# Optimization experiments

Measured on AMD Instinct MI355X. Metric: run time of the kernel, lower is better.

The kernel has to match this reference:

```python
import jax, jax.numpy as jnp
import numpy as np

N_NODES = 16500   # 100 battles x 165 hexes
N_EDGES = 100000  # per link type
K = 3             # number of link types (HeteroConv branches)
C_IN, C_HID, C_OUT = 170, 256, 256
GEN_EPS = 1e-7    # GENConv eps
BN_EPS = 1e-5     # BatchNorm1d eps


def setup_inputs() -> dict:
    key = jax.random.key(0)
    ki = iter(jax.random.split(key, 32))
    inp = {}
    inp["x"] = jax.random.normal(next(ki), (N_NODES, C_IN), jnp.float32)
    inp["edge_index"] = jax.random.randint(next(ki), (K, 2, N_EDGES), 0, N_NODES, dtype=jnp.int32)
    inp["edge_attr"] = jax.random.normal(next(ki), (K, N_EDGES, 1), jnp.float32)

    def uni(k, fan_in, shape):
        b = float(1.0 / np.sqrt(fan_in))
        return jax.random.uniform(k, shape, jnp.float32, -b, b)

    dims = [(C_IN, C_HID), (C_HID, C_HID), (C_HID, C_OUT)]
    for l, (ci, co) in enumerate(dims):
        inp[f"We{l}"] = uni(next(ki), 1, (K, 1, ci))          # edge encoder Linear(1, ci)
        inp[f"be{l}"] = jnp.zeros((K, ci), jnp.float32)
        inp[f"Wa{l}"] = uni(next(ki), ci, (K, ci, 2 * ci))     # MLP layer 1 (expansion=2)
        inp[f"ba{l}"] = jnp.zeros((K, 2 * ci), jnp.float32)
        inp[f"g{l}"] = jnp.ones((K, 2 * ci), jnp.float32)      # BatchNorm gamma
        inp[f"bt{l}"] = jnp.zeros((K, 2 * ci), jnp.float32)    # BatchNorm beta
        inp[f"Wb{l}"] = uni(next(ki), 2 * ci, (K, 2 * ci, co)) # MLP layer 2
        inp[f"bb{l}"] = jnp.zeros((K, co), jnp.float32)
    return inp


def _genconv(x, src, dst, ea, We, be, Wa, ba, g, bt, Wb, bb):
    """PyG GENConv (aggr='softmax', t=1, eps=1e-7, norm='batch') with self loops."""
    n = x.shape[0]
    loops = jnp.arange(n, dtype=src.dtype)
    src = jnp.concatenate([src, loops])
    dst = jnp.concatenate([dst, loops])
    ea = jnp.concatenate([ea, jnp.ones((n, ea.shape[1]), ea.dtype)], axis=0)
    e = ea @ We + be                           # [E+N, ci] edge encoder
    msg = jax.nn.relu(x[src] + e) + GEN_EPS    # [E+N, ci] message
    # per-destination, per-channel segment softmax aggregation
    mx = jax.ops.segment_max(msg, dst, num_segments=n)
    w = jnp.exp(msg - mx[dst])
    den = jax.ops.segment_sum(w, dst, num_segments=n)
    aggr = jax.ops.segment_sum(msg * w, dst, num_segments=n) / den
    out = aggr + x                             # residual with root node
    # MLP: Linear -> BatchNorm(train stats) -> ReLU -> Linear
    h = out @ Wa + ba
    mu = h.mean(axis=0)
    var = ((h - mu) ** 2).mean(axis=0)
    h = (h - mu) * jax.lax.rsqrt(var + BN_EPS) * g + bt
    h = jax.nn.relu(h)
    return h @ Wb + bb


_conv_k = jax.vmap(_genconv, in_axes=(None, 0, 0, 0, 0, 0, 0, 0, 0, 0, 0, 0))


def _forward(x, edge_index, edge_attr, layers):
    h = x
    for i, p in enumerate(layers):
        # HeteroConv: run GENConv per link type, sum-aggregate over types
        h = _conv_k(h, edge_index[:, 0], edge_index[:, 1], edge_attr, *p).sum(axis=0)
        if i < len(layers) - 1:
            h = jax.nn.leaky_relu(h, 0.01)
    return h


def reference(x, edge_index, edge_attr,
              We0, be0, Wa0, ba0, g0, bt0, Wb0, bb0,
              We1, be1, Wa1, ba1, g1, bt1, Wb1, bb1,
              We2, be2, Wa2, ba2, g2, bt2, Wb2, bb2):
    layers = [(We0, be0, Wa0, ba0, g0, bt0, Wb0, bb0),
              (We1, be1, Wa1, ba1, g1, bt1, Wb1, bb1),
              (We2, be2, Wa2, ba2, g2, bt2, Wb2, bb2)]
    return _forward(x, edge_index, edge_attr, layers)
```

## Files before the change

kernel.cpp:

```cpp
#include <hip/hip_runtime.h>
#include <math.h>

#define NN 16500
#define NP 16512
#define NE 100000
#define KT 3

typedef __attribute__((ext_vector_type(8))) short bf8_t;
typedef __attribute__((ext_vector_type(4))) float f4_t;

__device__ __forceinline__ unsigned short f2bf(float f) {
    unsigned int u = __float_as_uint(f);
    u += 0x7fffu + ((u >> 16) & 1u);
    return (unsigned short)(u >> 16);
}
__device__ __forceinline__ float bf2f(unsigned short h) {
    return __uint_as_float(((unsigned int)h) << 16);
}
__device__ __forceinline__ void gload16(unsigned short* lds, const unsigned short* g) {
    __builtin_amdgcn_global_load_lds(
        (const __attribute__((address_space(1))) void*)g,
        (__attribute__((address_space(3))) void*)lds, 16, 0, 0);
}


__global__ void deg_kernel(const int* __restrict__ ei, int* __restrict__ deg) {
    int t = blockIdx.x * blockDim.x + threadIdx.x;
    if (t >= KT * NE) return;
    int k = t / NE, e = t - k * NE;
    int d = ei[k * 2 * NE + NE + e];
    atomicAdd(&deg[k * NN + d], 1);
}

__global__ void scan_kernel(const int* __restrict__ deg, int* __restrict__ offs,
                            int* __restrict__ cursor) {
    int k = blockIdx.x;
    const int* dg = deg + k * NN;
    int* of = offs + k * (NN + 1);
    int* cu = cursor + k * NN;
    __shared__ int part[256];
    int tid = threadIdx.x;
    const int chunk = (NN + 255) / 256;
    int s0 = tid * chunk, s1 = min(NN, s0 + chunk);
    if (s0 > s1) s0 = s1;
    int sum = 0;
    for (int i = s0; i < s1; ++i) sum += dg[i];
    part[tid] = sum;
    __syncthreads();
    for (int off = 1; off < 256; off <<= 1) {
        int v = part[tid];
        int vp = (tid >= off) ? part[tid - off] : 0;
        __syncthreads();
        part[tid] = v + vp;
        __syncthreads();
    }
    int run = (tid == 0) ? 0 : part[tid - 1];
    for (int i = s0; i < s1; ++i) {
        of[i] = run; cu[i] = run;
        run += dg[i];
    }
    if (tid == 255) of[NN] = run;
}

__global__ void scatter_kernel(const int* __restrict__ ei, const float* __restrict__ ea,
                               int* __restrict__ cursor, int2* __restrict__ se) {
    int t = blockIdx.x * blockDim.x + threadIdx.x;
    if (t >= KT * NE) return;
    int k = t / NE, e = t - k * NE;
    int s = ei[k * 2 * NE + e];
    int d = ei[k * 2 * NE + NE + e];
    float a = ea[(size_t)k * NE + e];
    int pos = atomicAdd(&cursor[k * NN + d], 1);
    int2 p; p.x = s; p.y = __float_as_int(a);
    se[(size_t)k * NE + pos] = p;
}


template<int CI, bool BF16X>
__device__ __forceinline__ void loadrow4(float out[4], const void* xv, int s, int c0) {
    if (BF16X) {
        const unsigned short* xb = (const unsigned short*)xv;
        uint2 u = *(const uint2*)(xb + (size_t)s * CI + c0);
        out[0] = bf2f((unsigned short)(u.x & 0xffffu));
        out[1] = bf2f((unsigned short)(u.x >> 16));
        out[2] = bf2f((unsigned short)(u.y & 0xffffu));
        out[3] = bf2f((unsigned short)(u.y >> 16));
    } else {
        const float* p = (const float*)xv + (size_t)s * CI + c0;
        if (c0 + 4 <= CI) {
            float2 ab = *(const float2*)p;
            float2 cd = *(const float2*)(p + 2);
            out[0] = ab.x; out[1] = ab.y; out[2] = cd.x; out[3] = cd.y;
        } else {
            #pragma unroll
            for (int e = 0; e < 4; ++e) out[e] = (c0 + e < CI) ? p[e] : 0.f;
        }
    }
}

template<int CI, bool BF16X>
__global__ __launch_bounds__(256) void aggr_kernel(
    const void* __restrict__ xv, const int2* __restrict__ se_all,
    const int* __restrict__ offs_all,
    const float* __restrict__ We_all, const float* __restrict__ be_all,
    unsigned short* __restrict__ out_hi)
{
    constexpr int KP = (CI + 31) / 32 * 32;
    int k = blockIdx.y;
    int wv = threadIdx.x >> 6, lane = threadIdx.x & 63;
    int c0 = lane * 4;
    unsigned short* o = out_hi + (size_t)k * NP * KP;
    const int2*  se   = se_all + (size_t)k * NE;
    const int*   offs = offs_all + k * (NN + 1);
    const float* We   = We_all + (size_t)k * CI;
    const float* be   = be_all + (size_t)k * CI;

    constexpr bool ACT_ALL = (64 * 4 == KP) && (CI == KP);
    bool act = ACT_ALL || (c0 < CI);
    float w[4], b[4];
    #pragma unroll
    for (int e = 0; e < 4; ++e) {
        bool a = (c0 + e) < CI;
        w[e] = a ? We[c0 + e] : 0.f;
        b[e] = a ? be[c0 + e] : 0.f;
    }

    for (int it = 0; it < 4; ++it) {
        int d = blockIdx.x * 16 + it * 4 + wv;
        if (d >= NN) {
            if (c0 < KP) { uint2 z = {0u, 0u}; *(uint2*)(o + (size_t)d * KP + c0) = z; }
            continue;
        }
        float xd[4] = {0.f, 0.f, 0.f, 0.f};
        if (act) loadrow4<CI, BF16X>(xd, xv, d, c0);
        #pragma unroll
        for (int e = 0; e < 4; ++e) if ((c0 + e) >= CI) xd[e] = 0.f;

        float den[4], num[4];
        #pragma unroll
        for (int e = 0; e < 4; ++e) {
            float mg = fmaxf(xd[e] + w[e] + b[e], 0.f);
            float ex = __expf(mg);
            den[e] = ex;
            num[e] = mg * ex;
        }

        auto step = [&](const float xc[4], float a) {
            #pragma unroll
            for (int e = 0; e < 4; ++e) {
                float t = xc[e] + fmaf(a, w[e], b[e]);
                float mg = fmaxf(t, 0.f);
                float ex = __expf(mg);
                den[e] += ex;
                num[e] = fmaf(mg, ex, num[e]);
            }
        };

        int start = offs[d], end = offs[d + 1];
        for (int base = start; base < end; base += 64) {
            int cnt = min(64, end - base);
            int sv = 0; float av = 0.f;
            if (lane < cnt) {
                int2 p = se[base + lane];
                sv = p.x; av = __int_as_float(p.y);
            }
            float x0[4] = {0.f,0.f,0.f,0.f}, x1[4] = {0.f,0.f,0.f,0.f};
            float x2[4] = {0.f,0.f,0.f,0.f}, x3[4] = {0.f,0.f,0.f,0.f};
            {
                int sA = __shfl(sv, 0), sB = __shfl(sv, 1);
                int sC = __shfl(sv, 2), sD = __shfl(sv, 3);
                if (act)            loadrow4<CI, BF16X>(x0, xv, sA, c0);
                if (act && cnt > 1) loadrow4<CI, BF16X>(x1, xv, sB, c0);
                if (act && cnt > 2) loadrow4<CI, BF16X>(x2, xv, sC, c0);
                if (act && cnt > 3) loadrow4<CI, BF16X>(x3, xv, sD, c0);
            }
            int j = 0;
            for (; j + 3 < cnt; j += 4) {
                float a0 = __shfl(av, j),     a1 = __shfl(av, j + 1);
                float a2 = __shfl(av, j + 2), a3 = __shfl(av, j + 3);
                int s4 = __shfl(sv, (j + 4) & 63), s5 = __shfl(sv, (j + 5) & 63);
                int s6 = __shfl(sv, (j + 6) & 63), s7 = __shfl(sv, (j + 7) & 63);
                step(x0, a0);
                if (act && (j + 4) < cnt) loadrow4<CI, BF16X>(x0, xv, s4, c0);
                step(x1, a1);
                if (act && (j + 5) < cnt) loadrow4<CI, BF16X>(x1, xv, s5, c0);
                step(x2, a2);
                if (act && (j + 6) < cnt) loadrow4<CI, BF16X>(x2, xv, s6, c0);
                step(x3, a3);
                if (act && (j + 7) < cnt) loadrow4<CI, BF16X>(x3, xv, s7, c0);
            }
            if (j < cnt)     step(x0, __shfl(av, j));
            if (j + 1 < cnt) step(x1, __shfl(av, j + 1));
            if (j + 2 < cnt) step(x2, __shfl(av, j + 2));
        }
        if (c0 < KP) {
            unsigned short r[4];
            #pragma unroll
            for (int e = 0; e < 4; ++e) {
                float v = ((c0 + e) < CI) ? (num[e] / den[e] + xd[e]) : 0.f;
                r[e] = f2bf(v);
            }
            uint2 pk = {(unsigned)r[0] | ((unsigned)r[1] << 16),
                        (unsigned)r[2] | ((unsigned)r[3] << 16)};
            *(uint2*)(o + (size_t)d * KP + c0) = pk;
        }
    }
}


struct SplitJob { const float* W; unsigned short* out; int kdim, ndim, np_, kp; };
struct SplitJobs { SplitJob j[6]; };

__global__ void split_all_kernel(SplitJobs jobs) {
    SplitJob jb = jobs.j[blockIdx.z];
    int idx = blockIdx.x * 256 + threadIdx.x;
    int total = KT * jb.np_ * jb.kp;
    if (idx >= total) return;
    int k = idx / (jb.np_ * jb.kp);
    int rem = idx - k * jb.np_ * jb.kp;
    int n = rem / jb.kp;
    int kk = rem - n * jb.kp;
    float v = (n < jb.ndim && kk < jb.kdim) ? jb.W[((size_t)k * jb.kdim + kk) * jb.ndim + n] : 0.f;
    jb.out[idx] = f2bf(v);
}


__global__ __launch_bounds__(256, 3) void gemm1_mfma(
    const unsigned short* __restrict__ A_hi,
    const unsigned short* __restrict__ B_hi,
    const float* __restrict__ bias_all, unsigned short* __restrict__ C_all,
    float* __restrict__ psum,
    int KP, int ldc, int Mv, int Nv)
{
    __shared__ unsigned short Ah[2][128 * 32];
    __shared__ unsigned short Bh[2][128 * 32];

    int z = blockIdx.z;
    int gxT = gridDim.x, gyT = gridDim.y;
    int NHP = gxT * 128;
    const unsigned short* Ahg = A_hi + (size_t)z * NP * KP;
    const unsigned short* Bhg = B_hi + (size_t)z * NHP * KP;
    const float* bias = bias_all + (size_t)z * Nv;
    unsigned short* C = C_all + (size_t)z * NP * ldc;

    int tid = threadIdx.x;
    int w = tid >> 6, l = tid & 63;
    int bm = blockIdx.y * 128, bn = blockIdx.x * 128;
    int lane15 = l & 15, quad = l >> 4;
    int wm = (w >> 1) * 64, wn = (w & 1) * 64;
    int srow = l & 15;
    int scol = (l >> 4) * 8;

    f4_t acc[4][4];
    #pragma unroll
    for (int i = 0; i < 4; ++i)
        #pragma unroll
        for (int j = 0; j < 4; ++j) { f4_t zz = {0.f,0.f,0.f,0.f}; acc[i][j] = zz; }

    size_t aoff0 = (size_t)(bm + 32 * w +  0 + srow) * KP + scol;
    size_t aoff1 = (size_t)(bm + 32 * w + 16 + srow) * KP + scol;
    size_t boff0 = (size_t)(bn + 32 * w +  0 + srow) * KP + scol;
    size_t boff1 = (size_t)(bn + 32 * w + 16 + srow) * KP + scol;
    int rb0 = 32 * w, rb1 = 32 * w + 16;
    int ta = (w >> 1) * 4, tb = (w & 1) * 4;

    gload16(&Ah[0][rb0 * 32], Ahg + aoff0);
    gload16(&Ah[0][rb1 * 32], Ahg + aoff1);
    gload16(&Bh[0][rb0 * 32], Bhg + boff0);
    gload16(&Bh[0][rb1 * 32], Bhg + boff1);
    __syncthreads();

    int cur = 0;
    for (int k0 = 32; k0 < KP; k0 += 32) {
        int nxt = cur ^ 1;
        gload16(&Ah[nxt][rb0 * 32], Ahg + aoff0 + k0);
        gload16(&Ah[nxt][rb1 * 32], Ahg + aoff1 + k0);
        gload16(&Bh[nxt][rb0 * 32], Bhg + boff0 + k0);
        gload16(&Bh[nxt][rb1 * 32], Bhg + boff1 + k0);

        bf8_t fa[4], fb[4];
        #pragma unroll
        for (int i = 0; i < 4; ++i) {
            fa[i] = *(const bf8_t*)&Ah[cur][(ta + i) * 512 + l * 8];
            fb[i] = *(const bf8_t*)&Bh[cur][(tb + i) * 512 + l * 8];
        }
        #pragma unroll
        for (int i = 0; i < 4; ++i)
            #pragma unroll
            for (int j = 0; j < 4; ++j)
                acc[i][j] = __builtin_amdgcn_mfma_f32_16x16x32_bf16(fa[i], fb[j], acc[i][j], 0, 0, 0);
        __syncthreads();
        cur = nxt;
    }
    {
        bf8_t fa[4], fb[4];
        #pragma unroll
        for (int i = 0; i < 4; ++i) {
            fa[i] = *(const bf8_t*)&Ah[cur][(ta + i) * 512 + l * 8];
            fb[i] = *(const bf8_t*)&Bh[cur][(tb + i) * 512 + l * 8];
        }
        #pragma unroll
        for (int i = 0; i < 4; ++i)
            #pragma unroll
            for (int j = 0; j < 4; ++j)
                acc[i][j] = __builtin_amdgcn_mfma_f32_16x16x32_bf16(fa[i], fb[j], acc[i][j], 0, 0, 0);
    }

    #pragma unroll
    for (int j = 0; j < 4; ++j) {
        int c = bn + wn + j * 16 + lane15;
        float bc = (c < Nv) ? bias[c] : 0.f;
        float s1 = 0.f, s2 = 0.f;
        #pragma unroll
        for (int i = 0; i < 4; ++i) {
            #pragma unroll
            for (int r5 = 0; r5 < 4; ++r5) {
                int r = bm + wm + i * 16 + quad * 4 + r5;
                float v = acc[i][j][r5] + bc;
                unsigned short q = f2bf(v);
                if (r < Mv && c < Nv) C[(size_t)r * ldc + c] = q;
                bool ok = (r < NN) && (c < Nv);
                float vq = ok ? bf2f(q) : 0.f;
                s1 += vq;
                s2 = fmaf(vq, vq, s2);
            }
        }
        s1 += __shfl_xor(s1, 16); s2 += __shfl_xor(s2, 16);
        s1 += __shfl_xor(s1, 32); s2 += __shfl_xor(s2, 32);
        if (quad == 0) {
            int wrow = w >> 1;
            int col = wn + j * 16 + lane15;
            size_t o = ((((size_t)z * gyT + blockIdx.y) * gxT + blockIdx.x) * 2 + wrow) * 256 + col * 2;
            float2 st = {s1, s2};
            *(float2*)&psum[o] = st;
        }
    }
}


__global__ __launch_bounds__(256) void finalize_kernel(
    const float* __restrict__ psum,
    const float* __restrict__ g_all, const float* __restrict__ bt_all,
    float* __restrict__ scale_all, float* __restrict__ shift_all,
    int hid, int gxT)
{
    int z = blockIdx.x;
    int t64 = threadIdx.x & 63;
    int slice = threadIdx.x >> 6;
    int c = blockIdx.y * 64 + t64;
    __shared__ double rs1[4][64];
    __shared__ double rs2[4][64];
    double s1 = 0.0, s2 = 0.0;
    if (c < gxT * 128) {
        int gx = c >> 7, col = c & 127;
        for (int gy = slice; gy < NP / 128; gy += 4) {
            size_t base = (((size_t)z * (NP / 128) + gy) * gxT + gx) * 2 * 256 + col * 2;
            float2 a  = *(const float2*)&psum[base];
            float2 b2 = *(const float2*)&psum[base + 256];
            s1 += (double)a.x + b2.x;
            s2 += (double)a.y + b2.y;
        }
    }
    rs1[slice][t64] = s1;
    rs2[slice][t64] = s2;
    __syncthreads();
    if (slice == 0 && c < hid) {
        double S1 = rs1[0][t64] + rs1[1][t64] + rs1[2][t64] + rs1[3][t64];
        double S2 = rs2[0][t64] + rs2[1][t64] + rs2[2][t64] + rs2[3][t64];
        double mu = S1 / NN;
        double var = S2 / NN - mu * mu;
        if (var < 0.0) var = 0.0;
        float rs = (float)(1.0 / sqrt(var + 1e-5));
        float sc = rs * g_all[(size_t)z * hid + c];
        scale_all[(size_t)z * 512 + c] = sc;
        shift_all[(size_t)z * 512 + c] = bt_all[(size_t)z * hid + c] - (float)mu * sc;
    }
}


__device__ __forceinline__ bf8_t bnpack(uint4 hv, float4 s0, float4 s1,
                                        float4 t0, float4 t1, int ch0, int hid) {
    unsigned int uu[4] = {hv.x, hv.y, hv.z, hv.w};
    float ss[8] = {s0.x, s0.y, s0.z, s0.w, s1.x, s1.y, s1.z, s1.w};
    float tt[8] = {t0.x, t0.y, t0.z, t0.w, t1.x, t1.y, t1.z, t1.w};
    bf8_t r;
    #pragma unroll
    for (int e = 0; e < 8; ++e) {
        unsigned short hb = (e & 1) ? (unsigned short)(uu[e >> 1] >> 16)
                                    : (unsigned short)(uu[e >> 1] & 0xffffu);
        float x = bf2f(hb);
        float val = (ch0 + e < hid) ? fmaxf(fmaf(x, ss[e], tt[e]), 0.f) : 0.f;
        r[e] = (short)f2bf(val);
    }
    return r;
}

__global__ __launch_bounds__(256, 2) void gemm2_mfma(
    const unsigned short* __restrict__ h_all, const float* __restrict__ scale_all,
    const float* __restrict__ shift_all,
    const unsigned short* __restrict__ B_hi,
    const float* __restrict__ bb,
    float* __restrict__ outf, unsigned short* __restrict__ outb,
    int KP, int hid, int leaky, int as_bf16)
{
    __shared__ unsigned short Ah[2][64 * 32];
    __shared__ unsigned short Bh[2][128 * 32];

    int tid = threadIdx.x;
    int w = tid >> 6, l = tid & 63;
    int bm = blockIdx.y * 64, bn = blockIdx.x * 128;
    int lane15 = l & 15, quad = l >> 4;
    int wm = (w >> 1) * 32, wn = (w & 1) * 64;
    int srow = l & 15, scol = (l >> 4) * 8;

    const int KPZ = KP / 32;
    const int NIT = 3 * KPZ;

    f4_t acc[2][4];
    #pragma unroll
    for (int i = 0; i < 2; ++i)
        #pragma unroll
        for (int j = 0; j < 4; ++j) { f4_t zz = {0.f,0.f,0.f,0.f}; acc[i][j] = zz; }

    int rb0 = 32 * w, rb1 = 32 * w + 16;
    int ta = (w >> 1) * 2, tb = (w & 1) * 4;
    int grow = ((tid >> 6) << 4) + (tid & 15);
    int ccol = ((tid >> 4) & 3) * 8;

    size_t arow = (size_t)(bm + grow) * KP + ccol;
    size_t brow0 = (size_t)(bn + 32 * w + srow) * KP + scol;
    size_t brow1 = (size_t)(bn + 32 * w + 16 + srow) * KP + scol;

    {
        uint4 hv = *(const uint4*)(h_all + arow);
        gload16(&Bh[0][rb0 * 32], B_hi + brow0);
        gload16(&Bh[0][rb1 * 32], B_hi + brow1);
        const float* scl = scale_all + ccol;
        const float* shf = shift_all + ccol;
        float4 s0 = *(const float4*)scl, s1 = *(const float4*)(scl + 4);
        float4 t0 = *(const float4*)shf, t1 = *(const float4*)(shf + 4);
        *(bf8_t*)&Ah[0][tid * 8] = bnpack(hv, s0, s1, t0, t1, ccol, hid);
    }
    __syncthreads();

    int cur = 0;
    for (int it = 0; it < NIT; ++it) {
        int nit = it + 1;
        bool have = nit < NIT;
        int nxt = cur ^ 1;
        uint4 hv;
        float4 s0, s1, t0, t1;
        int nch = 0;
        if (have) {
            int nzz = nit / KPZ, nkk = (nit - nzz * KPZ) * 32;
            nch = nkk + ccol;
            hv = *(const uint4*)(h_all + (size_t)nzz * NP * KP + arow + nkk);
            const float* scl = scale_all + (size_t)nzz * 512 + nch;
            const float* shf = shift_all + (size_t)nzz * 512 + nch;
            s0 = *(const float4*)scl; s1 = *(const float4*)(scl + 4);
            t0 = *(const float4*)shf; t1 = *(const float4*)(shf + 4);
            const unsigned short* bz = B_hi + (size_t)nzz * 256 * KP + nkk;
            gload16(&Bh[nxt][rb0 * 32], bz + brow0);
            gload16(&Bh[nxt][rb1 * 32], bz + brow1);
        }
        bf8_t fa[2], fb[4];
        #pragma unroll
        for (int i = 0; i < 2; ++i)
            fa[i] = *(const bf8_t*)&Ah[cur][(ta + i) * 512 + l * 8];
        #pragma unroll
        for (int j = 0; j < 4; ++j)
            fb[j] = *(const bf8_t*)&Bh[cur][(tb + j) * 512 + l * 8];
        #pragma unroll
        for (int i = 0; i < 2; ++i)
            #pragma unroll
            for (int j = 0; j < 4; ++j)
                acc[i][j] = __builtin_amdgcn_mfma_f32_16x16x32_bf16(fa[i], fb[j], acc[i][j], 0, 0, 0);
        if (have)
            *(bf8_t*)&Ah[nxt][tid * 8] = bnpack(hv, s0, s1, t0, t1, nch, hid);
        __syncthreads();
        cur = nxt;
    }

    #pragma unroll
    for (int j = 0; j < 4; ++j) {
        int c = bn + wn + j * 16 + lane15;
        float bsum = bb[c] + bb[256 + c] + bb[512 + c];
        #pragma unroll
        for (int i = 0; i < 2; ++i) {
            #pragma unroll
            for (int r5 = 0; r5 < 4; ++r5) {
                int r = bm + wm + i * 16 + quad * 4 + r5;
                if (r < NN) {
                    float v = acc[i][j][r5] + bsum;
                    if (leaky) v = (v > 0.f) ? v : 0.01f * v;
                    if (as_bf16) outb[(size_t)r * 256 + c] = f2bf(v);
                    else         outf[(size_t)r * 256 + c] = v;
                }
            }
        }
    }
}


extern "C" void kernel_launch(void* const* d_in, const int* in_sizes, int n_in,
                              void* d_out, int out_size, void* d_ws, size_t ws_size,
                              hipStream_t stream)
{
    const float* x  = (const float*)d_in[0];
    const int*   ei = (const int*)d_in[1];
    const float* ea = (const float*)d_in[2];

    char* w = (char*)d_ws;
    auto alloc = [&](size_t bytes) {
        char* p = w;
        w += (bytes + 255) & ~(size_t)255;
        return p;
    };
    int* deg    = (int*)alloc((size_t)KT * NN * 4);
    int* offs   = (int*)alloc((size_t)KT * (NN + 1) * 4);
    int* cursor = (int*)alloc((size_t)KT * NN * 4);
    int2* se    = (int2*)alloc((size_t)KT * NE * 8);
    unsigned short* a1_hi = (unsigned short*)alloc((size_t)KT * NP * 256 * 2);
    unsigned short* h3 = (unsigned short*)alloc((size_t)KT * NP * 512 * 2);
    unsigned short* bta_l[3];
    unsigned short* btb_l[3];
    for (int l = 0; l < 3; ++l) {
        bta_l[l] = (unsigned short*)alloc((size_t)KT * 512 * 256 * 2);
        btb_l[l] = (unsigned short*)alloc((size_t)KT * 256 * 512 * 2);
    }
    float* psum = (float*)alloc((size_t)KT * (NP / 128) * 4 * 2 * 256 * 4);
    float* scale3 = (float*)alloc((size_t)KT * 512 * 4);
    float* shift3 = (float*)alloc((size_t)KT * 512 * 4);
    unsigned short* bufA = (unsigned short*)alloc((size_t)NN * 256 * 2);
    unsigned short* bufB = (unsigned short*)alloc((size_t)NN * 256 * 2);

    hipMemsetAsync(deg, 0, (size_t)KT * NN * 4, stream);
    int net = KT * NE;
    deg_kernel<<<(net + 255) / 256, 256, 0, stream>>>(ei, deg);
    scan_kernel<<<KT, 256, 0, stream>>>(deg, offs, cursor);
    scatter_kernel<<<(net + 255) / 256, 256, 0, stream>>>(ei, ea, cursor, se);

    SplitJobs jobs;
    int maxtot = 0;
    for (int l = 0; l < 3; ++l) {
        int ci  = (l == 0) ? 170 : 256;
        int KP1 = (ci + 31) / 32 * 32;
        int hid = 2 * ci;
        int NHP = (hid + 127) / 128 * 128;
        int KP2 = (hid + 31) / 32 * 32;
        jobs.j[2 * l]     = { (const float*)d_in[3 + 8 * l + 2], bta_l[l], ci,  hid, NHP, KP1 };
        jobs.j[2 * l + 1] = { (const float*)d_in[3 + 8 * l + 6], btb_l[l], hid, 256, 256, KP2 };
        maxtot = max(maxtot, KT * NHP * KP1);
        maxtot = max(maxtot, KT * 256 * KP2);
    }
    dim3 gsp((maxtot + 255) / 256, 1, 6);
    split_all_kernel<<<gsp, 256, 0, stream>>>(jobs);

    const void* hin = x;
    for (int l = 0; l < 3; ++l) {
        int ci  = (l == 0) ? 170 : 256;
        int KP1 = (ci + 31) / 32 * 32;
        int hid = 2 * ci;
        int NHP = (hid + 127) / 128 * 128;
        int KP2 = (hid + 31) / 32 * 32;
        const float* We = (const float*)d_in[3 + 8 * l + 0];
        const float* be = (const float*)d_in[3 + 8 * l + 1];
        const float* ba = (const float*)d_in[3 + 8 * l + 3];
        const float* g  = (const float*)d_in[3 + 8 * l + 4];
        const float* bt = (const float*)d_in[3 + 8 * l + 5];
        const float* bb = (const float*)d_in[3 + 8 * l + 7];

        dim3 ga(NP / 16, KT);
        if (l == 0)
            aggr_kernel<170, false><<<ga, 256, 0, stream>>>(hin, se, offs, We, be, a1_hi);
        else
            aggr_kernel<256, true><<<ga, 256, 0, stream>>>(hin, se, offs, We, be, a1_hi);

        dim3 g1(NHP / 128, NP / 128, KT);
        gemm1_mfma<<<g1, 256, 0, stream>>>(a1_hi, bta_l[l], ba, h3, psum, KP1, KP2, NN, hid);

        dim3 gf(KT, 8);
        finalize_kernel<<<gf, 256, 0, stream>>>(psum, g, bt, scale3, shift3, hid, NHP / 128);

        unsigned short* outb = (l == 0) ? bufA : bufB;
        dim3 g2(2, NP / 64);
        gemm2_mfma<<<g2, 256, 0, stream>>>(h3, scale3, shift3, btb_l[l], bb,
                                           (float*)d_out, outb, KP2, hid,
                                           (l < 2) ? 1 : 0, (l < 2) ? 1 : 0);

        hin = (l < 2) ? (const void*)outb : nullptr;
    }
}
```

Baseline: 671.2 us.

## Replace LDS-staged GEMM tiles with direct register loads of MFMA fragments

```diff
diff --git a/kernel.cpp b/kernel.cpp
--- a/kernel.cpp
+++ b/kernel.cpp
@@ -16,11 +16,6 @@
 }
 __device__ __forceinline__ float bf2f(unsigned short h) {
     return __uint_as_float(((unsigned int)h) << 16);
-}
-__device__ __forceinline__ void gload16(unsigned short* lds, const unsigned short* g) {
-    __builtin_amdgcn_global_load_lds(
-        (const __attribute__((address_space(1))) void*)g,
-        (__attribute__((address_space(3))) void*)lds, 16, 0, 0);
 }
 
 
@@ -230,110 +225,83 @@
     const unsigned short* __restrict__ B_hi,
     const float* __restrict__ bias_all, unsigned short* __restrict__ C_all,
     float* __restrict__ psum,
-    int KP, int ldc, int Mv, int Nv)
+    int KP, int ldc, int Nv)
 {
-    __shared__ unsigned short Ah[2][128 * 32];
-    __shared__ unsigned short Bh[2][128 * 32];
+    __shared__ float red[4][128][2];
 
     int z = blockIdx.z;
     int gxT = gridDim.x, gyT = gridDim.y;
     int NHP = gxT * 128;
-    const unsigned short* Ahg = A_hi + (size_t)z * NP * KP;
-    const unsigned short* Bhg = B_hi + (size_t)z * NHP * KP;
+    const unsigned short* A = A_hi + (size_t)z * NP * KP;
+    const unsigned short* B = B_hi + (size_t)z * NHP * KP;
     const float* bias = bias_all + (size_t)z * Nv;
     unsigned short* C = C_all + (size_t)z * NP * ldc;
 
-    int tid = threadIdx.x;
-    int w = tid >> 6, l = tid & 63;
-    int bm = blockIdx.y * 128, bn = blockIdx.x * 128;
-    int lane15 = l & 15, quad = l >> 4;
-    int wm = (w >> 1) * 64, wn = (w & 1) * 64;
-    int srow = l & 15;
-    int scol = (l >> 4) * 8;
-
-    f4_t acc[4][4];
-    #pragma unroll
-    for (int i = 0; i < 4; ++i)
-        #pragma unroll
-        for (int j = 0; j < 4; ++j) { f4_t zz = {0.f,0.f,0.f,0.f}; acc[i][j] = zz; }
-
-    size_t aoff0 = (size_t)(bm + 32 * w +  0 + srow) * KP + scol;
-    size_t aoff1 = (size_t)(bm + 32 * w + 16 + srow) * KP + scol;
-    size_t boff0 = (size_t)(bn + 32 * w +  0 + srow) * KP + scol;
-    size_t boff1 = (size_t)(bn + 32 * w + 16 + srow) * KP + scol;
-    int rb0 = 32 * w, rb1 = 32 * w + 16;
-    int ta = (w >> 1) * 4, tb = (w & 1) * 4;
-
-    gload16(&Ah[0][rb0 * 32], Ahg + aoff0);
-    gload16(&Ah[0][rb1 * 32], Ahg + aoff1);
-    gload16(&Bh[0][rb0 * 32], Bhg + boff0);
-    gload16(&Bh[0][rb1 * 32], Bhg + boff1);
-    __syncthreads();
-
-    int cur = 0;
-    for (int k0 = 32; k0 < KP; k0 += 32) {
-        int nxt = cur ^ 1;
-        gload16(&Ah[nxt][rb0 * 32], Ahg + aoff0 + k0);
-        gload16(&Ah[nxt][rb1 * 32], Ahg + aoff1 + k0);
-        gload16(&Bh[nxt][rb0 * 32], Bhg + boff0 + k0);
-        gload16(&Bh[nxt][rb1 * 32], Bhg + boff1 + k0);
-
-        bf8_t fa[4], fb[4];
-        #pragma unroll
-        for (int i = 0; i < 4; ++i) {
-            fa[i] = *(const bf8_t*)&Ah[cur][(ta + i) * 512 + l * 8];
-            fb[i] = *(const bf8_t*)&Bh[cur][(tb + i) * 512 + l * 8];
-        }
-        #pragma unroll
-        for (int i = 0; i < 4; ++i)
+    int tid = threadIdx.x, w = tid >> 6, l = tid & 63;
+    int bm = blockIdx.y * 64, bn = blockIdx.x * 128;
+    int lane15 = l & 15, quad = l >> 4, kc8 = quad * 8;
+
+    const unsigned short* ap = A + (size_t)(bm + w * 16 + lane15) * KP + kc8;
+    const unsigned short* bp = B + (size_t)(bn + lane15) * KP + kc8;
+    size_t bfs = (size_t)16 * KP;
+
+    int NK = KP / 32;
+
+    f4_t acc[8];
+    #pragma unroll
+    for (int cf = 0; cf < 8; ++cf) { f4_t zz = {0.f,0.f,0.f,0.f}; acc[cf] = zz; }
+
+    bf8_t a_c = *(const bf8_t*)ap;
+    bf8_t b_c[8];
+    #pragma unroll
+    for (int cf = 0; cf < 8; ++cf) b_c[cf] = *(const bf8_t*)(bp + cf * bfs);
+
+    for (int ks = 0; ks < NK; ++ks) {
+        bf8_t a_n, b_n[8];
+        if (ks + 1 < NK) {
+            int ko = (ks + 1) * 32;
+            a_n = *(const bf8_t*)(ap + ko);
             #pragma unroll
-            for (int j = 0; j < 4; ++j)
-                acc[i][j] = __builtin_amdgcn_mfma_f32_16x16x32_bf16(fa[i], fb[j], acc[i][j], 0, 0, 0);
-        __syncthreads();
-        cur = nxt;
-    }
-    {
-        bf8_t fa[4], fb[4];
-        #pragma unroll
-        for (int i = 0; i < 4; ++i) {
-            fa[i] = *(const bf8_t*)&Ah[cur][(ta + i) * 512 + l * 8];
-            fb[i] = *(const bf8_t*)&Bh[cur][(tb + i) * 512 + l * 8];
-        }
-        #pragma unroll
-        for (int i = 0; i < 4; ++i)
-            #pragma unroll
-            for (int j = 0; j < 4; ++j)
-                acc[i][j] = __builtin_amdgcn_mfma_f32_16x16x32_bf16(fa[i], fb[j], acc[i][j], 0, 0, 0);
-    }
-
-    #pragma unroll
-    for (int j = 0; j < 4; ++j) {
-        int c = bn + wn + j * 16 + lane15;
+            for (int cf = 0; cf < 8; ++cf) b_n[cf] = *(const bf8_t*)(bp + cf * bfs + ko);
+        }
+        #pragma unroll
+        for (int cf = 0; cf < 8; ++cf)
+            acc[cf] = __builtin_amdgcn_mfma_f32_16x16x32_bf16(a_c, b_c[cf], acc[cf], 0, 0, 0);
+        a_c = a_n;
+        #pragma unroll
+        for (int cf = 0; cf < 8; ++cf) b_c[cf] = b_n[cf];
+    }
+
+    #pragma unroll
+    for (int cf = 0; cf < 8; ++cf) {
+        int c = bn + cf * 16 + lane15;
         float bc = (c < Nv) ? bias[c] : 0.f;
         float s1 = 0.f, s2 = 0.f;
         #pragma unroll
-        for (int i = 0; i < 4; ++i) {
-            #pragma unroll
-            for (int r5 = 0; r5 < 4; ++r5) {
-                int r = bm + wm + i * 16 + quad * 4 + r5;
-                float v = acc[i][j][r5] + bc;
-                unsigned short q = f2bf(v);
-                if (r < Mv && c < Nv) C[(size_t)r * ldc + c] = q;
-                bool ok = (r < NN) && (c < Nv);
-                float vq = ok ? bf2f(q) : 0.f;
-                s1 += vq;
-                s2 = fmaf(vq, vq, s2);
-            }
+        for (int r5 = 0; r5 < 4; ++r5) {
+            int r = bm + w * 16 + quad * 4 + r5;
+            float v = acc[cf][r5] + bc;
+            unsigned short q = f2bf(v);
+            bool ok = (r < NN) && (c < Nv);
+            if (ok) C[(size_t)r * ldc + c] = q;
+            float vq = ok ? bf2f(q) : 0.f;
+            s1 += vq;
+            s2 = fmaf(vq, vq, s2);
         }
         s1 += __shfl_xor(s1, 16); s2 += __shfl_xor(s2, 16);
         s1 += __shfl_xor(s1, 32); s2 += __shfl_xor(s2, 32);
         if (quad == 0) {
-            int wrow = w >> 1;
-            int col = wn + j * 16 + lane15;
-            size_t o = ((((size_t)z * gyT + blockIdx.y) * gxT + blockIdx.x) * 2 + wrow) * 256 + col * 2;
-            float2 st = {s1, s2};
-            *(float2*)&psum[o] = st;
-        }
+            red[w][cf * 16 + lane15][0] = s1;
+            red[w][cf * 16 + lane15][1] = s2;
+        }
+    }
+    __syncthreads();
+    if (tid < 128) {
+        float S1 = red[0][tid][0] + red[1][tid][0] + red[2][tid][0] + red[3][tid][0];
+        float S2 = red[0][tid][1] + red[1][tid][1] + red[2][tid][1] + red[3][tid][1];
+        size_t o = (((size_t)z * gyT + blockIdx.y) * gxT + blockIdx.x) * 256 + tid * 2;
+        psum[o] = S1;
+        psum[o + 1] = S2;
     }
 }
 
@@ -348,17 +316,16 @@
     int t64 = threadIdx.x & 63;
     int slice = threadIdx.x >> 6;
     int c = blockIdx.y * 64 + t64;
+    const int NBY = NP / 64;
     __shared__ double rs1[4][64];
     __shared__ double rs2[4][64];
     double s1 = 0.0, s2 = 0.0;
     if (c < gxT * 128) {
         int gx = c >> 7, col = c & 127;
-        for (int gy = slice; gy < NP / 128; gy += 4) {
-            size_t base = (((size_t)z * (NP / 128) + gy) * gxT + gx) * 2 * 256 + col * 2;
-            float2 a  = *(const float2*)&psum[base];
-            float2 b2 = *(const float2*)&psum[base + 256];
-            s1 += (double)a.x + b2.x;
-            s2 += (double)a.y + b2.y;
+        for (int by = slice; by < NBY; by += 4) {
+            size_t base = (((size_t)z * NBY + by) * gxT + gx) * 256 + col * 2;
+            s1 += (double)psum[base];
+            s2 += (double)psum[base + 1];
         }
     }
     rs1[slice][t64] = s1;
@@ -378,24 +345,26 @@
 }
 
 
-__device__ __forceinline__ bf8_t bnpack(uint4 hv, float4 s0, float4 s1,
-                                        float4 t0, float4 t1, int ch0, int hid) {
-    unsigned int uu[4] = {hv.x, hv.y, hv.z, hv.w};
+__device__ __forceinline__ bf8_t bnpack8(bf8_t a, const float* __restrict__ scl,
+                                         const float* __restrict__ shf,
+                                         int nch, int hid) {
+    float4 s0 = *(const float4*)(scl + nch);
+    float4 s1 = *(const float4*)(scl + nch + 4);
+    float4 t0 = *(const float4*)(shf + nch);
+    float4 t1 = *(const float4*)(shf + nch + 4);
     float ss[8] = {s0.x, s0.y, s0.z, s0.w, s1.x, s1.y, s1.z, s1.w};
     float tt[8] = {t0.x, t0.y, t0.z, t0.w, t1.x, t1.y, t1.z, t1.w};
     bf8_t r;
     #pragma unroll
     for (int e = 0; e < 8; ++e) {
-        unsigned short hb = (e & 1) ? (unsigned short)(uu[e >> 1] >> 16)
-                                    : (unsigned short)(uu[e >> 1] & 0xffffu);
-        float x = bf2f(hb);
-        float val = (ch0 + e < hid) ? fmaxf(fmaf(x, ss[e], tt[e]), 0.f) : 0.f;
+        float x = bf2f((unsigned short)a[e]);
+        float val = (nch + e < hid) ? fmaxf(fmaf(x, ss[e], tt[e]), 0.f) : 0.f;
         r[e] = (short)f2bf(val);
     }
     return r;
 }
 
-__global__ __launch_bounds__(256, 2) void gemm2_mfma(
+__global__ __launch_bounds__(256, 3) void gemm2_mfma(
     const unsigned short* __restrict__ h_all, const float* __restrict__ scale_all,
     const float* __restrict__ shift_all,
     const unsigned short* __restrict__ B_hi,
@@ -403,99 +372,59 @@
     float* __restrict__ outf, unsigned short* __restrict__ outb,
     int KP, int hid, int leaky, int as_bf16)
 {
-    __shared__ unsigned short Ah[2][64 * 32];
-    __shared__ unsigned short Bh[2][128 * 32];
-
-    int tid = threadIdx.x;
-    int w = tid >> 6, l = tid & 63;
+    int tid = threadIdx.x, w = tid >> 6, l = tid & 63;
     int bm = blockIdx.y * 64, bn = blockIdx.x * 128;
-    int lane15 = l & 15, quad = l >> 4;
-    int wm = (w >> 1) * 32, wn = (w & 1) * 64;
-    int srow = l & 15, scol = (l >> 4) * 8;
-
-    const int KPZ = KP / 32;
-    const int NIT = 3 * KPZ;
-
-    f4_t acc[2][4];
-    #pragma unroll
-    for (int i = 0; i < 2; ++i)
-        #pragma unroll
-        for (int j = 0; j < 4; ++j) { f4_t zz = {0.f,0.f,0.f,0.f}; acc[i][j] = zz; }
-
-    int rb0 = 32 * w, rb1 = 32 * w + 16;
-    int ta = (w >> 1) * 2, tb = (w & 1) * 4;
-    int grow = ((tid >> 6) << 4) + (tid & 15);
-    int ccol = ((tid >> 4) & 3) * 8;
-
-    size_t arow = (size_t)(bm + grow) * KP + ccol;
-    size_t brow0 = (size_t)(bn + 32 * w + srow) * KP + scol;
-    size_t brow1 = (size_t)(bn + 32 * w + 16 + srow) * KP + scol;
-
-    {
-        uint4 hv = *(const uint4*)(h_all + arow);
-        gload16(&Bh[0][rb0 * 32], B_hi + brow0);
-        gload16(&Bh[0][rb1 * 32], B_hi + brow1);
-        const float* scl = scale_all + ccol;
-        const float* shf = shift_all + ccol;
-        float4 s0 = *(const float4*)scl, s1 = *(const float4*)(scl + 4);
-        float4 t0 = *(const float4*)shf, t1 = *(const float4*)(shf + 4);
-        *(bf8_t*)&Ah[0][tid * 8] = bnpack(hv, s0, s1, t0, t1, ccol, hid);
-    }
-    __syncthreads();
-
-    int cur = 0;
+    int lane15 = l & 15, quad = l >> 4, kc8 = quad * 8;
+
+    const unsigned short* hp = h_all + (size_t)(bm + w * 16 + lane15) * KP + kc8;
+    const unsigned short* bp = B_hi + (size_t)(bn + lane15) * KP + kc8;
+    size_t bfs = (size_t)16 * KP;
+
+    int NK = KP / 32, NIT = 3 * NK;
+
+    f4_t acc[8];
+    #pragma unroll
+    for (int cf = 0; cf < 8; ++cf) { f4_t zz = {0.f,0.f,0.f,0.f}; acc[cf] = zz; }
+
+    bf8_t a_c = *(const bf8_t*)hp;
+    bf8_t b_c[8];
+    #pragma unroll
+    for (int cf = 0; cf < 8; ++cf) b_c[cf] = *(const bf8_t*)(bp + cf * bfs);
+
+    int zc = 0, kk = 0;
     for (int it = 0; it < NIT; ++it) {
-        int nit = it + 1;
-        bool have = nit < NIT;
-        int nxt = cur ^ 1;
-        uint4 hv;
-        float4 s0, s1, t0, t1;
-        int nch = 0;
-        if (have) {
-            int nzz = nit / KPZ, nkk = (nit - nzz * KPZ) * 32;
-            nch = nkk + ccol;
-            hv = *(const uint4*)(h_all + (size_t)nzz * NP * KP + arow + nkk);
-            const float* scl = scale_all + (size_t)nzz * 512 + nch;
-            const float* shf = shift_all + (size_t)nzz * 512 + nch;
-            s0 = *(const float4*)scl; s1 = *(const float4*)(scl + 4);
-            t0 = *(const float4*)shf; t1 = *(const float4*)(shf + 4);
-            const unsigned short* bz = B_hi + (size_t)nzz * 256 * KP + nkk;
-            gload16(&Bh[nxt][rb0 * 32], bz + brow0);
-            gload16(&Bh[nxt][rb1 * 32], bz + brow1);
-        }
-        bf8_t fa[2], fb[4];
-        #pragma unroll
-        for (int i = 0; i < 2; ++i)
-            fa[i] = *(const bf8_t*)&Ah[cur][(ta + i) * 512 + l * 8];
-        #pragma unroll
-        for (int j = 0; j < 4; ++j)
-            fb[j] = *(const bf8_t*)&Bh[cur][(tb + j) * 512 + l * 8];
-        #pragma unroll
-        for (int i = 0; i < 2; ++i)
+        int zn = zc, kn = kk + 32;
+        if (kn == KP) { kn = 0; zn = zc + 1; }
+        bf8_t a_n, b_n[8];
+        if (it + 1 < NIT) {
+            a_n = *(const bf8_t*)(hp + (size_t)zn * NP * KP + kn);
+            const unsigned short* bz = bp + (size_t)zn * 256 * KP + kn;
             #pragma unroll
-            for (int j = 0; j < 4; ++j)
-                acc[i][j] = __builtin_amdgcn_mfma_f32_16x16x32_bf16(fa[i], fb[j], acc[i][j], 0, 0, 0);
-        if (have)
-            *(bf8_t*)&Ah[nxt][tid * 8] = bnpack(hv, s0, s1, t0, t1, nch, hid);
-        __syncthreads();
-        cur = nxt;
-    }
-
-    #pragma unroll
-    for (int j = 0; j < 4; ++j) {
-        int c = bn + wn + j * 16 + lane15;
+            for (int cf = 0; cf < 8; ++cf) b_n[cf] = *(const bf8_t*)(bz + cf * bfs);
+        }
+        int nch = kk + kc8;
+        bf8_t fa = bnpack8(a_c, scale_all + zc * 512, shift_all + zc * 512, nch, hid);
+        #pragma unroll
+        for (int cf = 0; cf < 8; ++cf)
+            acc[cf] = __builtin_amdgcn_mfma_f32_16x16x32_bf16(fa, b_c[cf], acc[cf], 0, 0, 0);
+        a_c = a_n;
+        #pragma unroll
+        for (int cf = 0; cf < 8; ++cf) b_c[cf] = b_n[cf];
+        zc = zn; kk = kn;
+    }
+
+    #pragma unroll
+    for (int cf = 0; cf < 8; ++cf) {
+        int c = bn + cf * 16 + lane15;
         float bsum = bb[c] + bb[256 + c] + bb[512 + c];
         #pragma unroll
-        for (int i = 0; i < 2; ++i) {
-            #pragma unroll
-            for (int r5 = 0; r5 < 4; ++r5) {
-                int r = bm + wm + i * 16 + quad * 4 + r5;
-                if (r < NN) {
-                    float v = acc[i][j][r5] + bsum;
-                    if (leaky) v = (v > 0.f) ? v : 0.01f * v;
-                    if (as_bf16) outb[(size_t)r * 256 + c] = f2bf(v);
-                    else         outf[(size_t)r * 256 + c] = v;
-                }
+        for (int r5 = 0; r5 < 4; ++r5) {
+            int r = bm + w * 16 + quad * 4 + r5;
+            if (r < NN) {
+                float v = acc[cf][r5] + bsum;
+                if (leaky) v = (v > 0.f) ? v : 0.01f * v;
+                if (as_bf16) outb[(size_t)r * 256 + c] = f2bf(v);
+                else         outf[(size_t)r * 256 + c] = v;
             }
         }
     }
@@ -528,7 +457,7 @@
         bta_l[l] = (unsigned short*)alloc((size_t)KT * 512 * 256 * 2);
         btb_l[l] = (unsigned short*)alloc((size_t)KT * 256 * 512 * 2);
     }
-    float* psum = (float*)alloc((size_t)KT * (NP / 128) * 4 * 2 * 256 * 4);
+    float* psum = (float*)alloc((size_t)KT * (NP / 64) * 4 * 256 * 4);
     float* scale3 = (float*)alloc((size_t)KT * 512 * 4);
     float* shift3 = (float*)alloc((size_t)KT * 512 * 4);
     unsigned short* bufA = (unsigned short*)alloc((size_t)NN * 256 * 2);
@@ -576,8 +505,8 @@
         else
             aggr_kernel<256, true><<<ga, 256, 0, stream>>>(hin, se, offs, We, be, a1_hi);
 
-        dim3 g1(NHP / 128, NP / 128, KT);
-        gemm1_mfma<<<g1, 256, 0, stream>>>(a1_hi, bta_l[l], ba, h3, psum, KP1, KP2, NN, hid);
+        dim3 g1(NHP / 128, NP / 64, KT);
+        gemm1_mfma<<<g1, 256, 0, stream>>>(a1_hi, bta_l[l], ba, h3, psum, KP1, KP2, hid);
 
         dim3 gf(KT, 8);
         finalize_kernel<<<gf, 256, 0, stream>>>(psum, g, bt, scale3, shift3, hid, NHP / 128);
```

New measurement: 1.114 ms. 1.66x slower.

## Deepen GEMM pipelines with 4-slot LDS ring and direct-to-LDS BN-on-read

Applied to the files above, without the earlier changes.

```diff
diff --git a/kernel.cpp b/kernel.cpp
--- a/kernel.cpp
+++ b/kernel.cpp
@@ -21,6 +21,11 @@
     __builtin_amdgcn_global_load_lds(
         (const __attribute__((address_space(1))) void*)g,
         (__attribute__((address_space(3))) void*)lds, 16, 0, 0);
+}
+__device__ __forceinline__ void pipe_barrier() {
+    __builtin_amdgcn_s_barrier();
+    __builtin_amdgcn_sched_barrier(0);
+    asm volatile("" ::: "memory");
 }
 
 
@@ -225,15 +230,17 @@
 }
 
 
-__global__ __launch_bounds__(256, 3) void gemm1_mfma(
+template<int KP>
+__global__ __launch_bounds__(256, 2) void gemm1_mfma(
     const unsigned short* __restrict__ A_hi,
     const unsigned short* __restrict__ B_hi,
     const float* __restrict__ bias_all, unsigned short* __restrict__ C_all,
-    float* __restrict__ psum,
-    int KP, int ldc, int Mv, int Nv)
+    float* __restrict__ psum, int ldc, int Nv)
 {
-    __shared__ unsigned short Ah[2][128 * 32];
-    __shared__ unsigned short Bh[2][128 * 32];
+    constexpr int NK = KP / 32;
+    constexpr int SLOT = 128 * 32;
+    __shared__ unsigned short Ah[4 * SLOT];
+    __shared__ unsigned short Bh[4 * SLOT];
 
     int z = blockIdx.z;
     int gxT = gridDim.x, gyT = gridDim.y;
@@ -243,13 +250,18 @@
     const float* bias = bias_all + (size_t)z * Nv;
     unsigned short* C = C_all + (size_t)z * NP * ldc;
 
-    int tid = threadIdx.x;
-    int w = tid >> 6, l = tid & 63;
+    int tid = threadIdx.x, w = tid >> 6, l = tid & 63;
     int bm = blockIdx.y * 128, bn = blockIdx.x * 128;
     int lane15 = l & 15, quad = l >> 4;
     int wm = (w >> 1) * 64, wn = (w & 1) * 64;
-    int srow = l & 15;
-    int scol = (l >> 4) * 8;
+    int srow = l & 15, scol = quad * 8;
+
+    size_t aoff0 = (size_t)(bm + 32 * w + srow) * KP + scol;
+    size_t aoff1 = aoff0 + (size_t)16 * KP;
+    size_t boff0 = (size_t)(bn + 32 * w + srow) * KP + scol;
+    size_t boff1 = boff0 + (size_t)16 * KP;
+    int rb0 = (2 * w) * 512, rb1 = (2 * w + 1) * 512;
+    int ta = (w >> 1) * 4, tb = (w & 1) * 4;
 
     f4_t acc[4][4];
     #pragma unroll
@@ -257,53 +269,34 @@
         #pragma unroll
         for (int j = 0; j < 4; ++j) { f4_t zz = {0.f,0.f,0.f,0.f}; acc[i][j] = zz; }
 
-    size_t aoff0 = (size_t)(bm + 32 * w +  0 + srow) * KP + scol;
-    size_t aoff1 = (size_t)(bm + 32 * w + 16 + srow) * KP + scol;
-    size_t boff0 = (size_t)(bn + 32 * w +  0 + srow) * KP + scol;
-    size_t boff1 = (size_t)(bn + 32 * w + 16 + srow) * KP + scol;
-    int rb0 = 32 * w, rb1 = 32 * w + 16;
-    int ta = (w >> 1) * 4, tb = (w & 1) * 4;
-
-    gload16(&Ah[0][rb0 * 32], Ahg + aoff0);
-    gload16(&Ah[0][rb1 * 32], Ahg + aoff1);
-    gload16(&Bh[0][rb0 * 32], Bhg + boff0);
-    gload16(&Bh[0][rb1 * 32], Bhg + boff1);
-    __syncthreads();
-
-    int cur = 0;
-    for (int k0 = 32; k0 < KP; k0 += 32) {
-        int nxt = cur ^ 1;
-        gload16(&Ah[nxt][rb0 * 32], Ahg + aoff0 + k0);
-        gload16(&Ah[nxt][rb1 * 32], Ahg + aoff1 + k0);
-        gload16(&Bh[nxt][rb0 * 32], Bhg + boff0 + k0);
-        gload16(&Bh[nxt][rb1 * 32], Bhg + boff1 + k0);
-
+    auto stage = [&](int t, int s) {
+        int k0 = t * 32;
+        gload16(&Ah[s * SLOT + rb0], Ahg + aoff0 + k0);
+        gload16(&Ah[s * SLOT + rb1], Ahg + aoff1 + k0);
+        gload16(&Bh[s * SLOT + rb0], Bhg + boff0 + k0);
+        gload16(&Bh[s * SLOT + rb1], Bhg + boff1 + k0);
+    };
+    stage(0, 0);
+    stage(1, 1);
+
+    #pragma unroll
+    for (int i = 0; i < NK; ++i) {
+        stage(min(i + 2, NK - 1), (i + 2) & 3);
+        asm volatile("s_waitcnt vmcnt(8)" ::: "memory");
+        pipe_barrier();
+        const unsigned short* As = &Ah[(i & 3) * SLOT];
+        const unsigned short* Bs = &Bh[(i & 3) * SLOT];
         bf8_t fa[4], fb[4];
         #pragma unroll
-        for (int i = 0; i < 4; ++i) {
-            fa[i] = *(const bf8_t*)&Ah[cur][(ta + i) * 512 + l * 8];
-            fb[i] = *(const bf8_t*)&Bh[cur][(tb + i) * 512 + l * 8];
-        }
-        #pragma unroll
-        for (int i = 0; i < 4; ++i)
+        for (int q = 0; q < 4; ++q) {
+            fa[q] = *(const bf8_t*)&As[(ta + q) * 512 + l * 8];
+            fb[q] = *(const bf8_t*)&Bs[(tb + q) * 512 + l * 8];
+        }
+        #pragma unroll
+        for (int q = 0; q < 4; ++q)
             #pragma unroll
             for (int j = 0; j < 4; ++j)
-                acc[i][j] = __builtin_amdgcn_mfma_f32_16x16x32_bf16(fa[i], fb[j], acc[i][j], 0, 0, 0);
-        __syncthreads();
-        cur = nxt;
-    }
-    {
-        bf8_t fa[4], fb[4];
-        #pragma unroll
-        for (int i = 0; i < 4; ++i) {
-            fa[i] = *(const bf8_t*)&Ah[cur][(ta + i) * 512 + l * 8];
-            fb[i] = *(const bf8_t*)&Bh[cur][(tb + i) * 512 + l * 8];
-        }
-        #pragma unroll
-        for (int i = 0; i < 4; ++i)
-            #pragma unroll
-            for (int j = 0; j < 4; ++j)
-                acc[i][j] = __builtin_amdgcn_mfma_f32_16x16x32_bf16(fa[i], fb[j], acc[i][j], 0, 0, 0);
+                acc[q][j] = __builtin_amdgcn_mfma_f32_16x16x32_bf16(fa[q], fb[j], acc[q][j], 0, 0, 0);
     }
 
     #pragma unroll
@@ -318,8 +311,8 @@
                 int r = bm + wm + i * 16 + quad * 4 + r5;
                 float v = acc[i][j][r5] + bc;
                 unsigned short q = f2bf(v);
-                if (r < Mv && c < Nv) C[(size_t)r * ldc + c] = q;
                 bool ok = (r < NN) && (c < Nv);
+                if (ok) C[(size_t)r * ldc + c] = q;
                 float vq = ok ? bf2f(q) : 0.f;
                 s1 += vq;
                 s2 = fmaf(vq, vq, s2);
@@ -378,43 +371,52 @@
 }
 
 
-__device__ __forceinline__ bf8_t bnpack(uint4 hv, float4 s0, float4 s1,
-                                        float4 t0, float4 t1, int ch0, int hid) {
-    unsigned int uu[4] = {hv.x, hv.y, hv.z, hv.w};
-    float ss[8] = {s0.x, s0.y, s0.z, s0.w, s1.x, s1.y, s1.z, s1.w};
-    float tt[8] = {t0.x, t0.y, t0.z, t0.w, t1.x, t1.y, t1.z, t1.w};
-    bf8_t r;
-    #pragma unroll
-    for (int e = 0; e < 8; ++e) {
-        unsigned short hb = (e & 1) ? (unsigned short)(uu[e >> 1] >> 16)
-                                    : (unsigned short)(uu[e >> 1] & 0xffffu);
-        float x = bf2f(hb);
-        float val = (ch0 + e < hid) ? fmaxf(fmaf(x, ss[e], tt[e]), 0.f) : 0.f;
-        r[e] = (short)f2bf(val);
-    }
-    return r;
-}
-
+template<int KP>
 __global__ __launch_bounds__(256, 2) void gemm2_mfma(
     const unsigned short* __restrict__ h_all, const float* __restrict__ scale_all,
     const float* __restrict__ shift_all,
     const unsigned short* __restrict__ B_hi,
     const float* __restrict__ bb,
     float* __restrict__ outf, unsigned short* __restrict__ outb,
-    int KP, int hid, int leaky, int as_bf16)
+    int hid, int leaky, int as_bf16)
 {
-    __shared__ unsigned short Ah[2][64 * 32];
-    __shared__ unsigned short Bh[2][128 * 32];
-
-    int tid = threadIdx.x;
-    int w = tid >> 6, l = tid & 63;
+    constexpr int NK = KP / 32;
+    constexpr int NIT = 3 * NK;
+    constexpr int ASLOT = 64 * 32;
+    constexpr int BSLOT = 128 * 32;
+    __shared__ unsigned short Ah[4 * ASLOT];
+    __shared__ unsigned short Bh[4 * BSLOT];
+    __shared__ __align__(16) float sclS[KT * 512];
+    __shared__ __align__(16) float shfS[KT * 512];
+
+    int tid = threadIdx.x, w = tid >> 6, l = tid & 63;
     int bm = blockIdx.y * 64, bn = blockIdx.x * 128;
     int lane15 = l & 15, quad = l >> 4;
     int wm = (w >> 1) * 32, wn = (w & 1) * 64;
-    int srow = l & 15, scol = (l >> 4) * 8;
-
-    const int KPZ = KP / 32;
-    const int NIT = 3 * KPZ;
+    int srow = l & 15, scol = quad * 8;
+    int ta = (w >> 1) * 2, tb = (w & 1) * 4;
+
+    size_t ao  = (size_t)(bm + 16 * w + srow) * KP + scol;
+    size_t bo0 = (size_t)(bn + 32 * w + srow) * KP + scol;
+    size_t bo1 = bo0 + (size_t)16 * KP;
+    int adst = w * 512;
+    int bdst0 = (2 * w) * 512, bdst1 = (2 * w + 1) * 512;
+
+    for (int idx = tid; idx < KT * 512; idx += 256) {
+        sclS[idx] = scale_all[idx];
+        shfS[idx] = shift_all[idx];
+    }
+    auto stage = [&](int t, int s) {
+        int zz = t / NK, kk = (t - zz * NK) * 32;
+        const unsigned short* hz = h_all + (size_t)zz * NP * KP + kk;
+        const unsigned short* bz = B_hi + (size_t)zz * 256 * KP + kk;
+        gload16(&Ah[s * ASLOT + adst], hz + ao);
+        gload16(&Bh[s * BSLOT + bdst0], bz + bo0);
+        gload16(&Bh[s * BSLOT + bdst1], bz + bo1);
+    };
+    stage(0, 0);
+    stage(1, 1);
+    __syncthreads();
 
     f4_t acc[2][4];
     #pragma unroll
@@ -422,63 +424,42 @@
         #pragma unroll
         for (int j = 0; j < 4; ++j) { f4_t zz = {0.f,0.f,0.f,0.f}; acc[i][j] = zz; }
 
-    int rb0 = 32 * w, rb1 = 32 * w + 16;
-    int ta = (w >> 1) * 2, tb = (w & 1) * 4;
-    int grow = ((tid >> 6) << 4) + (tid & 15);
-    int ccol = ((tid >> 4) & 3) * 8;
-
-    size_t arow = (size_t)(bm + grow) * KP + ccol;
-    size_t brow0 = (size_t)(bn + 32 * w + srow) * KP + scol;
-    size_t brow1 = (size_t)(bn + 32 * w + 16 + srow) * KP + scol;
-
-    {
-        uint4 hv = *(const uint4*)(h_all + arow);
-        gload16(&Bh[0][rb0 * 32], B_hi + brow0);
-        gload16(&Bh[0][rb1 * 32], B_hi + brow1);
-        const float* scl = scale_all + ccol;
-        const float* shf = shift_all + ccol;
+    #pragma unroll 4
+    for (int i = 0; i < NIT; ++i) {
+        stage(min(i + 2, NIT - 1), (i + 2) & 3);
+        asm volatile("s_waitcnt vmcnt(6)" ::: "memory");
+        pipe_barrier();
+        int zz = i / NK, kk = (i - zz * NK) * 32;
+        int chb = kk + quad * 8;
+        const float* scl = &sclS[zz * 512 + chb];
+        const float* shf = &shfS[zz * 512 + chb];
         float4 s0 = *(const float4*)scl, s1 = *(const float4*)(scl + 4);
         float4 t0 = *(const float4*)shf, t1 = *(const float4*)(shf + 4);
-        *(bf8_t*)&Ah[0][tid * 8] = bnpack(hv, s0, s1, t0, t1, ccol, hid);
-    }
-    __syncthreads();
-
-    int cur = 0;
-    for (int it = 0; it < NIT; ++it) {
-        int nit = it + 1;
-        bool have = nit < NIT;
-        int nxt = cur ^ 1;
-        uint4 hv;
-        float4 s0, s1, t0, t1;
-        int nch = 0;
-        if (have) {
-            int nzz = nit / KPZ, nkk = (nit - nzz * KPZ) * 32;
-            nch = nkk + ccol;
-            hv = *(const uint4*)(h_all + (size_t)nzz * NP * KP + arow + nkk);
-            const float* scl = scale_all + (size_t)nzz * 512 + nch;
-            const float* shf = shift_all + (size_t)nzz * 512 + nch;
-            s0 = *(const float4*)scl; s1 = *(const float4*)(scl + 4);
-            t0 = *(const float4*)shf; t1 = *(const float4*)(shf + 4);
-            const unsigned short* bz = B_hi + (size_t)nzz * 256 * KP + nkk;
-            gload16(&Bh[nxt][rb0 * 32], bz + brow0);
-            gload16(&Bh[nxt][rb1 * 32], bz + brow1);
-        }
-        bf8_t fa[2], fb[4];
-        #pragma unroll
-        for (int i = 0; i < 2; ++i)
-            fa[i] = *(const bf8_t*)&Ah[cur][(ta + i) * 512 + l * 8];
-        #pragma unroll
-        for (int j = 0; j < 4; ++j)
-            fb[j] = *(const bf8_t*)&Bh[cur][(tb + j) * 512 + l * 8];
-        #pragma unroll
-        for (int i = 0; i < 2; ++i)
-            #pragma unroll
-            for (int j = 0; j < 4; ++j)
-                acc[i][j] = __builtin_amdgcn_mfma_f32_16x16x32_bf16(fa[i], fb[j], acc[i][j], 0, 0, 0);
-        if (have)
-            *(bf8_t*)&Ah[nxt][tid * 8] = bnpack(hv, s0, s1, t0, t1, nch, hid);
-        __syncthreads();
-        cur = nxt;
+        float ss[8] = {s0.x, s0.y, s0.z, s0.w, s1.x, s1.y, s1.z, s1.w};
+        float tt[8] = {t0.x, t0.y, t0.z, t0.w, t1.x, t1.y, t1.z, t1.w};
+        const unsigned short* As = &Ah[(i & 3) * ASLOT];
+        const unsigned short* Bs = &Bh[(i & 3) * BSLOT];
+        bf8_t far0 = *(const bf8_t*)&As[(ta + 0) * 512 + l * 8];
+        bf8_t far1 = *(const bf8_t*)&As[(ta + 1) * 512 + l * 8];
+        bf8_t fb[4];
+        #pragma unroll
+        for (int j = 0; j < 4; ++j) fb[j] = *(const bf8_t*)&Bs[(tb + j) * 512 + l * 8];
+        bf8_t fa0, fa1;
+        #pragma unroll
+        for (int e = 0; e < 8; ++e) {
+            bool okc = (chb + e) < hid;
+            float x0 = bf2f((unsigned short)far0[e]);
+            float x1 = bf2f((unsigned short)far1[e]);
+            float v0 = okc ? fmaxf(fmaf(x0, ss[e], tt[e]), 0.f) : 0.f;
+            float v1 = okc ? fmaxf(fmaf(x1, ss[e], tt[e]), 0.f) : 0.f;
+            fa0[e] = (short)f2bf(v0);
+            fa1[e] = (short)f2bf(v1);
+        }
+        #pragma unroll
+        for (int j = 0; j < 4; ++j) {
+            acc[0][j] = __builtin_amdgcn_mfma_f32_16x16x32_bf16(fa0, fb[j], acc[0][j], 0, 0, 0);
+            acc[1][j] = __builtin_amdgcn_mfma_f32_16x16x32_bf16(fa1, fb[j], acc[1][j], 0, 0, 0);
+        }
     }
 
     #pragma unroll
@@ -486,12 +467,12 @@
         int c = bn + wn + j * 16 + lane15;
         float bsum = bb[c] + bb[256 + c] + bb[512 + c];
         #pragma unroll
-        for (int i = 0; i < 2; ++i) {
+        for (int i2 = 0; i2 < 2; ++i2) {
             #pragma unroll
             for (int r5 = 0; r5 < 4; ++r5) {
-                int r = bm + wm + i * 16 + quad * 4 + r5;
+                int r = bm + wm + i2 * 16 + quad * 4 + r5;
                 if (r < NN) {
-                    float v = acc[i][j][r5] + bsum;
+                    float v = acc[i2][j][r5] + bsum;
                     if (leaky) v = (v > 0.f) ? v : 0.01f * v;
                     if (as_bf16) outb[(size_t)r * 256 + c] = f2bf(v);
                     else         outf[(size_t)r * 256 + c] = v;
@@ -547,7 +528,7 @@
         int KP1 = (ci + 31) / 32 * 32;
         int hid = 2 * ci;
         int NHP = (hid + 127) / 128 * 128;
-        int KP2 = (hid + 31) / 32 * 32;
+        int KP2 = (hid + 63) / 64 * 64;
         jobs.j[2 * l]     = { (const float*)d_in[3 + 8 * l + 2], bta_l[l], ci,  hid, NHP, KP1 };
         jobs.j[2 * l + 1] = { (const float*)d_in[3 + 8 * l + 6], btb_l[l], hid, 256, 256, KP2 };
         maxtot = max(maxtot, KT * NHP * KP1);
@@ -562,7 +543,7 @@
         int KP1 = (ci + 31) / 32 * 32;
         int hid = 2 * ci;
         int NHP = (hid + 127) / 128 * 128;
-        int KP2 = (hid + 31) / 32 * 32;
+        int KP2 = (hid + 63) / 64 * 64;
         const float* We = (const float*)d_in[3 + 8 * l + 0];
         const float* be = (const float*)d_in[3 + 8 * l + 1];
         const float* ba = (const float*)d_in[3 + 8 * l + 3];
@@ -577,16 +558,24 @@
             aggr_kernel<256, true><<<ga, 256, 0, stream>>>(hin, se, offs, We, be, a1_hi);
 
         dim3 g1(NHP / 128, NP / 128, KT);
-        gemm1_mfma<<<g1, 256, 0, stream>>>(a1_hi, bta_l[l], ba, h3, psum, KP1, KP2, NN, hid);
+        if (l == 0)
+            gemm1_mfma<192><<<g1, 256, 0, stream>>>(a1_hi, bta_l[l], ba, h3, psum, KP2, hid);
+        else
+            gemm1_mfma<256><<<g1, 256, 0, stream>>>(a1_hi, bta_l[l], ba, h3, psum, KP2, hid);
 
         dim3 gf(KT, 8);
         finalize_kernel<<<gf, 256, 0, stream>>>(psum, g, bt, scale3, shift3, hid, NHP / 128);
 
         unsigned short* outb = (l == 0) ? bufA : bufB;
         dim3 g2(2, NP / 64);
-        gemm2_mfma<<<g2, 256, 0, stream>>>(h3, scale3, shift3, btb_l[l], bb,
-                                           (float*)d_out, outb, KP2, hid,
-                                           (l < 2) ? 1 : 0, (l < 2) ? 1 : 0);
+        if (l == 0)
+            gemm2_mfma<384><<<g2, 256, 0, stream>>>(h3, scale3, shift3, btb_l[l], bb,
+                                                    (float*)d_out, outb, hid,
+                                                    1, 1);
+        else
+            gemm2_mfma<512><<<g2, 256, 0, stream>>>(h3, scale3, shift3, btb_l[l], bb,
+                                                    (float*)d_out, outb, hid,
+                                                    (l < 2) ? 1 : 0, (l < 2) ? 1 : 0);
 
         hin = (l < 2) ? (const void*)outb : nullptr;
     }
```

Result: slower. 798.4 us (+19.0%).
